# Kernel optimization log

Hardware: AMD Instinct MI355X
Metric: run time of the kernel (lower is better)

Reference implementation:

```python
import jax, jax.numpy as jnp
import numpy as np

NB_CLASSES = 10
NB_NEIGHBORS = 75  # 1 closest + 74 precomputed geodesic neighbors


def setup_inputs() -> dict:
    key = jax.random.key(0)
    k0, k1, k2, k3, k4, k5 = jax.random.split(key, 6)
    nb_data, nb_train, d = 1024, 100000, 256
    x = jax.random.normal(k0, (nb_data, d), dtype=jnp.float32)
    X = jax.random.normal(k1, (nb_train, d), dtype=jnp.float32)
    # train table is stored normalized + centered (init_nn_querier)
    X = X / jnp.linalg.norm(X, axis=1, keepdims=True)
    X = X - jnp.mean(X, axis=0)
    center = jax.random.normal(k2, (d,), dtype=jnp.float32) * 0.01
    train_labels = jax.random.randint(k3, (nb_train,), 0, NB_CLASSES).astype(jnp.int32)
    train_neighbor_index = jax.random.randint(
        k4, (nb_train, NB_NEIGHBORS - 1), 0, nb_train).astype(jnp.int32)
    cali_nonconformity = jnp.sort(
        jax.random.randint(k5, (1000,), 0, NB_NEIGHBORS)).astype(jnp.int32)
    return {
        "x": x, "X": X, "center": center,
        "train_labels": train_labels,
        "train_neighbor_index": train_neighbor_index,
        "cali_nonconformity": cali_nonconformity,
    }


def reference(x, X, center, train_labels, train_neighbor_index, cali_nonconformity):
    # --- find_train_knns: normalize query, center, closest-neighbor search ---
    xq = x / jnp.linalg.norm(x, axis=1, keepdims=True) - center  # [B, d]
    # squared euclidean distances to every train point: [B, nb_train]
    d2 = (jnp.sum(xq * xq, axis=1, keepdims=True)
          - 2.0 * (xq @ X.T)
          + jnp.sum(X * X, axis=1)[None, :])
    closest = jnp.argmin(d2, axis=1)                               # [B]
    # neighbor list = closest point prepended to its precomputed table row
    neigh = jnp.concatenate(
        [closest[:, None], train_neighbor_index[closest]], axis=1)  # [B, K]
    knns_labels = train_labels[neigh]                              # [B, K]
    # --- nonconformity: per-class bincount, #knns NOT in class ---
    counts = jnp.sum(jax.nn.one_hot(knns_labels, NB_CLASSES, dtype=jnp.int32),
                     axis=1)                                       # [B, C]
    knns_not_in_class = jnp.sum(counts, axis=1, keepdims=True) - counts
    # --- preds_conf_cred: conformal p-values via bisect_left ---
    nb_cali = cali_nonconformity.shape[0]
    pos = jnp.searchsorted(cali_nonconformity, knns_not_in_class, side='left')
    p_value = (nb_cali - pos).astype(jnp.float32) / float(nb_cali)  # [B, C]
    preds = jnp.argmax(p_value, axis=1)                             # [B]
    top2, _ = jax.lax.top_k(p_value, 2)                             # [B, 2]
    nb_data = p_value.shape[0]
    creds = jnp.zeros_like(p_value).at[jnp.arange(nb_data), preds].set(top2[:, 0])
    return creds
```

## Files before the change

### kernel.cpp

```cpp
#include <hip/hip_runtime.h>
#include <stdint.h>


typedef __attribute__((ext_vector_type(8))) short short8;
typedef __attribute__((ext_vector_type(4))) float float4v;

static __device__ __forceinline__ unsigned short bf16_rn(float f) {
    unsigned int u = __float_as_uint(f);
    unsigned int r = (u + 0x7FFFu + ((u >> 16) & 1u)) >> 16;
    return (unsigned short)r;
}

static __device__ __forceinline__ void gload_lds16(const void* g, void* l) {
    __builtin_amdgcn_global_load_lds(
        (const __attribute__((address_space(1))) unsigned int*)g,
        (__attribute__((address_space(3))) unsigned int*)l, 16, 0, 0);
}

__global__ void prep_all(const float* __restrict__ X, const float* __restrict__ x,
                         const float* __restrict__ center,
                         unsigned short* __restrict__ Bh, unsigned short* __restrict__ Bl,
                         float* __restrict__ xn2,
                         unsigned short* __restrict__ Ah, unsigned short* __restrict__ Al,
                         float* __restrict__ q2, unsigned long long* __restrict__ gkey,
                         int nb_train, int Np, int B, int Mp) {
    const int tid = threadIdx.x;
    const int tb = Np >> 2;
    if (blockIdx.x < (unsigned)tb) {
        int row = blockIdx.x * 4 + (tid >> 6);
        int lane = tid & 63;
        if (row >= nb_train) {
            ushort4 z = make_ushort4(0, 0, 0, 0);
            *(ushort4*)(Bh + (size_t)row * 256 + lane * 4) = z;
            *(ushort4*)(Bl + (size_t)row * 256 + lane * 4) = z;
            if (lane == 0) xn2[row] = 3.0e38f;
            return;
        }
        float4 v = ((const float4*)(X + (size_t)row * 256))[lane];
        ushort4 h, l;
        h.x = bf16_rn(v.x); l.x = bf16_rn(v.x - __uint_as_float((unsigned)h.x << 16));
        h.y = bf16_rn(v.y); l.y = bf16_rn(v.y - __uint_as_float((unsigned)h.y << 16));
        h.z = bf16_rn(v.z); l.z = bf16_rn(v.z - __uint_as_float((unsigned)h.z << 16));
        h.w = bf16_rn(v.w); l.w = bf16_rn(v.w - __uint_as_float((unsigned)h.w << 16));
        *(ushort4*)(Bh + (size_t)row * 256 + lane * 4) = h;
        *(ushort4*)(Bl + (size_t)row * 256 + lane * 4) = l;
        float ss = v.x * v.x + v.y * v.y + v.z * v.z + v.w * v.w;
        #pragma unroll
        for (int s = 1; s < 64; s <<= 1) ss += __shfl_xor(ss, s);
        if (lane == 0) xn2[row] = ss;
        return;
    }
    int row = blockIdx.x - tb;
    if (row >= Mp) return;
    if (tid == 0) gkey[row] = ~0ULL;
    if (row >= B) {
        Ah[(size_t)row * 256 + tid] = 0;
        Al[(size_t)row * 256 + tid] = 0;
        if (tid == 0) q2[row] = 0.0f;
        return;
    }
    float v = x[(size_t)row * 256 + tid];
    float ss = v * v;
    #pragma unroll
    for (int s = 1; s < 64; s <<= 1) ss += __shfl_xor(ss, s);
    __shared__ float partial[4];
    __shared__ float partial2[4];
    if ((tid & 63) == 0) partial[tid >> 6] = ss;
    __syncthreads();
    float tot = partial[0] + partial[1] + partial[2] + partial[3];
    float inv = 1.0f / sqrtf(tot);
    float val = v * inv - center[tid];
    unsigned short hb = bf16_rn(val);
    float hf = __uint_as_float((unsigned int)hb << 16);
    unsigned short lb = bf16_rn(val - hf);
    Ah[(size_t)row * 256 + tid] = hb;
    Al[(size_t)row * 256 + tid] = lb;
    float ss2 = val * val;
    #pragma unroll
    for (int s = 1; s < 64; s <<= 1) ss2 += __shfl_xor(ss2, s);
    if ((tid & 63) == 0) partial2[tid >> 6] = ss2;
    __syncthreads();
    if (tid == 0) q2[row] = partial2[0] + partial2[1] + partial2[2] + partial2[3];
}

__global__ __launch_bounds__(256, 4) void mfma_tile(
    const unsigned short* __restrict__ Adata,
    const unsigned short* __restrict__ Bdata,
    const float* __restrict__ q2, const float* __restrict__ xn2,
    unsigned long long* __restrict__ gkey,
    int Mp, int Np, int nb_train, int B,
    int ntiles, int nper, int mtiles)
{
    __shared__ unsigned short As[128 * 64];
    __shared__ unsigned short Bs[128 * 64];
    __shared__ unsigned long long skey[128];

    const int bid = blockIdx.x;
    const int xcd = bid & 7;
    const int s_  = bid >> 3;
    const int n_t = xcd * nper + (s_ / mtiles);
    const int m_t = s_ - (s_ / mtiles) * mtiles;
    if (n_t >= ntiles) return;
    const int mtile = m_t * 128;
    const int ntile = n_t * 128;

    const int tid  = threadIdx.x;
    const int wave = tid >> 6;
    const int lane = tid & 63;

    if (tid < 128) skey[tid] = ~0ULL;

    const int isB   = wave >> 1;
    const int Rwave = (wave & 1) * 64;
    const int lrow8  = lane >> 3;
    const int lchunk = lane & 7;
    const size_t APROD = (size_t)Mp * 256;
    const size_t BPROD = (size_t)Np * 256;
    const unsigned short* sbase = isB
        ? (Bdata + (size_t)(ntile + Rwave + lrow8) * 256 + (size_t)((lchunk ^ lrow8) * 8))
        : (Adata + (size_t)(mtile + Rwave + lrow8) * 256 + (size_t)((lchunk ^ lrow8) * 8));
    unsigned short* lwave = (isB ? Bs : As) + Rwave * 64;

    const int mq = (wave >> 1) * 64;
    const int nq = (wave & 1) * 64;
    const int lrow = lane & 15;
    const int kseg = lane >> 4;
    const int sw = lrow & 7;

    float4v acc[4][4];
    #pragma unroll
    for (int i = 0; i < 4; ++i)
        #pragma unroll
        for (int j = 0; j < 4; ++j)
            acc[i][j] = (float4v){0.f, 0.f, 0.f, 0.f};

    for (int s = 0; s < 12; ++s) {
        const int phase = s >> 2;
        const int sk = (s & 3) * 64;
        size_t srcOff = (size_t)sk;
        if (!isB) { if (phase == 1) srcOff += APROD; }
        else      { if (phase == 2) srcOff += BPROD; }
        const unsigned short* g = sbase + srcOff;
        __syncthreads();
        #pragma unroll
        for (int q = 0; q < 8; ++q)
            gload_lds16(g + q * 2048, lwave + q * 512);
        __syncthreads();
        #pragma unroll
        for (int t = 0; t < 2; ++t) {
            const int wch = ((t * 4 + kseg) ^ sw) * 8;
            short8 a[4], b[4];
            #pragma unroll
            for (int i = 0; i < 4; ++i)
                a[i] = *(const short8*)&As[(mq + i * 16 + lrow) * 64 + wch];
            #pragma unroll
            for (int j = 0; j < 4; ++j)
                b[j] = *(const short8*)&Bs[(nq + j * 16 + lrow) * 64 + wch];
            #pragma unroll
            for (int i = 0; i < 4; ++i)
                #pragma unroll
                for (int j = 0; j < 4; ++j)
                    acc[i][j] = __builtin_amdgcn_mfma_f32_16x16x32_bf16(
                        a[i], b[j], acc[i][j], 0, 0, 0);
        }
    }

    float xnv[4];
    #pragma unroll
    for (int j = 0; j < 4; ++j)
        xnv[j] = xn2[ntile + nq + j * 16 + lrow];

    #pragma unroll
    for (int i = 0; i < 4; ++i) {
        #pragma unroll
        for (int r = 0; r < 4; ++r) {
            const int lm = mq + i * 16 + kseg * 4 + r;
            const int mi = mtile + lm;
            unsigned long long best = ~0ULL;
            if (mi < B) {
                float q2v = q2[mi];
                #pragma unroll
                for (int j = 0; j < 4; ++j) {
                    int t_ = ntile + nq + j * 16 + lrow;
                    float sc = fmaxf(q2v - 2.0f * acc[i][j][r] + xnv[j], 0.0f);
                    unsigned long long key =
                        ((unsigned long long)__float_as_uint(sc) << 32) | (unsigned int)t_;
                    best = (key < best) ? key : best;
                }
            }
            #pragma unroll
            for (int sft = 1; sft < 16; sft <<= 1) {
                unsigned long long o = __shfl_xor(best, sft);
                best = (o < best) ? o : best;
            }
            if (lrow == 0 && mi < B) atomicMin(&skey[lm], best);
        }
    }
    __syncthreads();
    if (tid < 128) {
        int mi = mtile + tid;
        if (mi < B && skey[tid] != ~0ULL) atomicMin(gkey + mi, skey[tid]);
    }
}

__global__ void classify(const unsigned long long* __restrict__ gkey,
                         const int* __restrict__ labels,
                         const int* __restrict__ nbr,
                         const int* __restrict__ cali,
                         float* __restrict__ out,
                         int knm1, int nb_cali, int B)
{
    int q = blockIdx.x * 4 + (threadIdx.x >> 6);
    int lane = threadIdx.x & 63;
    if (q >= B) return;
    int closest = (int)(gkey[q] & 0xFFFFFFFFULL);
    int K = knm1 + 1;
    int lbl0 = -1, lbl1 = -1;
    if (lane < K) {
        int idx = (lane == 0) ? closest : nbr[(size_t)closest * knm1 + (lane - 1)];
        lbl0 = labels[idx];
    }
    int j2 = lane + 64;
    if (j2 < K) {
        int idx = nbr[(size_t)closest * knm1 + (j2 - 1)];
        lbl1 = labels[idx];
    }
    int bestc = 0, bestp = -1;
    #pragma unroll
    for (int c = 0; c < 10; ++c) {
        int cnt = __popcll(__ballot(lbl0 == c)) + __popcll(__ballot(lbl1 == c));
        int v = K - cnt;
        int lo = 0, hi = nb_cali;
        while (lo < hi) {
            int mid = (lo + hi) >> 1;
            if (cali[mid] < v) lo = mid + 1; else hi = mid;
        }
        int p = nb_cali - lo;
        if (p > bestp) { bestp = p; bestc = c; }
    }
    float pv = (float)bestp / (float)nb_cali;
    if (lane < 10)
        out[(size_t)q * 10 + lane] = (lane == bestc) ? pv : 0.0f;
}

extern "C" void kernel_launch(void* const* d_in, const int* in_sizes, int n_in,
                              void* d_out, int out_size, void* d_ws, size_t ws_size,
                              hipStream_t stream) {
    const float* x      = (const float*)d_in[0];
    const float* X      = (const float*)d_in[1];
    const float* center = (const float*)d_in[2];
    const int* labels   = (const int*)d_in[3];
    const int* nbr      = (const int*)d_in[4];
    const int* cali     = (const int*)d_in[5];
    float* out = (float*)d_out;

    const int d        = in_sizes[2];
    const int B        = in_sizes[0] / d;
    const int nb_train = in_sizes[3];
    const int knm1     = in_sizes[4] / nb_train;
    const int nb_cali  = in_sizes[5];

    const int Mp = (B + 127) & ~127;
    const int Np = (nb_train + 127) & ~127;

    char* ws = (char*)d_ws;
    size_t off = 0;
    unsigned long long* gkey = (unsigned long long*)(ws + off); off += (size_t)Mp * 8;
    unsigned short* Adata = (unsigned short*)(ws + off); off += (size_t)Mp * 256 * 2 * 2;
    float* q2 = (float*)(ws + off); off += (size_t)Mp * 4;
    unsigned short* Bdata = (unsigned short*)(ws + off); off += (size_t)Np * 256 * 2 * 2;
    float* xn2 = (float*)(ws + off); off += (size_t)Np * 4;

    unsigned short* Ah = Adata;
    unsigned short* Al = Adata + (size_t)Mp * 256;
    unsigned short* Bh = Bdata;
    unsigned short* Bl = Bdata + (size_t)Np * 256;

    prep_all<<<Np / 4 + Mp, 256, 0, stream>>>(X, x, center, Bh, Bl, xn2,
                                              Ah, Al, q2, gkey,
                                              nb_train, Np, B, Mp);
    const int ntiles = Np / 128;
    const int mtiles = Mp / 128;
    const int nper   = (ntiles + 7) / 8;
    mfma_tile<<<8 * nper * mtiles, 256, 0, stream>>>(
        Adata, Bdata, q2, xn2, gkey, Mp, Np, nb_train, B, ntiles, nper, mtiles);
    classify<<<(B + 3) / 4, 256, 0, stream>>>(gkey, labels, nbr, cali, out,
                                              knm1, nb_cali, B);
}
```

Before: 378.6 us.

## Rework distance GEMM into 256x256 tiles with double-buffered LDS pipeline

The MFMA distance kernel moves from 128x128 tiles with 256 threads to 256x256 tiles with 512 threads. Global-to-LDS loads are double-buffered and interleaved with MFMA phases using explicit waitcnt, barriers and setprio, so that memory traffic overlaps compute and each loaded operand is reused more. The M dimension is hardwired to four 256-row tiles, which only covers batches of up to 1024 queries. The roughly 128KB of LDS per block limits occupancy.

```diff
diff --git a/kernel.cpp b/kernel.cpp
--- a/kernel.cpp
+++ b/kernel.cpp
@@ -4,6 +4,11 @@
 
 typedef __attribute__((ext_vector_type(8))) short short8;
 typedef __attribute__((ext_vector_type(4))) float float4v;
+
+#define BAR()   asm volatile("s_barrier" ::: "memory")
+#define LGKM0() asm volatile("s_waitcnt lgkmcnt(0)" ::: "memory")
+#define VMC6()  asm volatile("s_waitcnt vmcnt(6)" ::: "memory")
+#define VMC0()  asm volatile("s_waitcnt vmcnt(0)" ::: "memory")
 
 static __device__ __forceinline__ unsigned short bf16_rn(float f) {
     unsigned int u = __float_as_uint(f);
@@ -83,106 +88,137 @@
     if (tid == 0) q2[row] = partial2[0] + partial2[1] + partial2[2] + partial2[3];
 }
 
-__global__ __launch_bounds__(256, 4) void mfma_tile(
+__global__ __launch_bounds__(512, 2) void mfma_tile(
     const unsigned short* __restrict__ Adata,
     const unsigned short* __restrict__ Bdata,
     const float* __restrict__ q2, const float* __restrict__ xn2,
     unsigned long long* __restrict__ gkey,
-    int Mp, int Np, int nb_train, int B,
-    int ntiles, int nper, int mtiles)
+    int Mp, int Np, int B, int ntiles)
 {
-    __shared__ unsigned short As[128 * 64];
-    __shared__ unsigned short Bs[128 * 64];
-    __shared__ unsigned long long skey[128];
-
-    const int bid = blockIdx.x;
-    const int xcd = bid & 7;
-    const int s_  = bid >> 3;
-    const int n_t = xcd * nper + (s_ / mtiles);
-    const int m_t = s_ - (s_ / mtiles) * mtiles;
-    if (n_t >= ntiles) return;
-    const int mtile = m_t * 128;
-    const int ntile = n_t * 128;
+    __shared__ unsigned short As[2][256 * 64];
+    __shared__ unsigned short Bs[2][256 * 64];
+
+    const int nwg  = ntiles * 4;
+    const int orig = blockIdx.x;
+    const int xcd  = orig & 7;
+    const int qq   = nwg >> 3, rr = nwg & 7;
+    const int wgid = (xcd < rr ? xcd * (qq + 1) : rr * (qq + 1) + (xcd - rr) * qq)
+                   + (orig >> 3);
+    const int mtile = (wgid & 3) * 256;
+    const int ntile = (wgid >> 2) * 256;
 
     const int tid  = threadIdx.x;
     const int wave = tid >> 6;
     const int lane = tid & 63;
-
-    if (tid < 128) skey[tid] = ~0ULL;
-
-    const int isB   = wave >> 1;
-    const int Rwave = (wave & 1) * 64;
-    const int lrow8  = lane >> 3;
-    const int lchunk = lane & 7;
     const size_t APROD = (size_t)Mp * 256;
     const size_t BPROD = (size_t)Np * 256;
-    const unsigned short* sbase = isB
-        ? (Bdata + (size_t)(ntile + Rwave + lrow8) * 256 + (size_t)((lchunk ^ lrow8) * 8))
-        : (Adata + (size_t)(mtile + Rwave + lrow8) * 256 + (size_t)((lchunk ^ lrow8) * 8));
-    unsigned short* lwave = (isB ? Bs : As) + Rwave * 64;
-
-    const int mq = (wave >> 1) * 64;
-    const int nq = (wave & 1) * 64;
-    const int lrow = lane & 15;
-    const int kseg = lane >> 4;
-    const int sw = lrow & 7;
-
-    float4v acc[4][4];
-    #pragma unroll
-    for (int i = 0; i < 4; ++i)
+
+    const int    srow = lane >> 3;
+    const int    schk = ((lane & 7) ^ srow) * 8;
+    const size_t aoff = (size_t)(mtile + wave * 8 + srow) * 256 + schk;
+    const size_t boff = (size_t)(ntile + wave * 8 + srow) * 256 + schk;
+    const int    dwav = wave * 512;
+
+    auto stageA = [&](int tt, int hh) {
+        if (tt >= 12) return;
+        const int p = tt >> 2, sk = (tt & 3) * 64;
+        const unsigned short* src = Adata + (p == 1 ? APROD : 0)
+                                  + aoff + (size_t)hh * (128 * 256) + sk;
+        unsigned short* dst = &As[tt & 1][hh * 8192 + dwav];
+        gload_lds16(src, dst);
+        gload_lds16(src + 64 * 256, dst + 4096);
+    };
+    auto stageB = [&](int tt, int hh) {
+        if (tt >= 12) return;
+        const int p = tt >> 2, sk = (tt & 3) * 64;
+        const unsigned short* src = Bdata + (p == 2 ? BPROD : 0)
+                                  + boff + (size_t)hh * (128 * 256) + sk;
+        unsigned short* dst = &Bs[tt & 1][hh * 8192 + dwav];
+        gload_lds16(src, dst);
+        gload_lds16(src + 64 * 256, dst + 4096);
+    };
+
+    const int wm = wave >> 2, wn = wave & 3;
+    const int lrow = lane & 15, kseg = lane >> 4, sw = lane & 7;
+    const int AM = wm * 128, BN = wn * 64;
+
+    float4v acc[8][4];
+    #pragma unroll
+    for (int i = 0; i < 8; ++i)
         #pragma unroll
         for (int j = 0; j < 4; ++j)
             acc[i][j] = (float4v){0.f, 0.f, 0.f, 0.f};
 
-    for (int s = 0; s < 12; ++s) {
-        const int phase = s >> 2;
-        const int sk = (s & 3) * 64;
-        size_t srcOff = (size_t)sk;
-        if (!isB) { if (phase == 1) srcOff += APROD; }
-        else      { if (phase == 2) srcOff += BPROD; }
-        const unsigned short* g = sbase + srcOff;
-        __syncthreads();
-        #pragma unroll
-        for (int q = 0; q < 8; ++q)
-            gload_lds16(g + q * 2048, lwave + q * 512);
-        __syncthreads();
-        #pragma unroll
-        for (int t = 0; t < 2; ++t) {
-            const int wch = ((t * 4 + kseg) ^ sw) * 8;
-            short8 a[4], b[4];
-            #pragma unroll
-            for (int i = 0; i < 4; ++i)
-                a[i] = *(const short8*)&As[(mq + i * 16 + lrow) * 64 + wch];
-            #pragma unroll
-            for (int j = 0; j < 4; ++j)
-                b[j] = *(const short8*)&Bs[(nq + j * 16 + lrow) * 64 + wch];
-            #pragma unroll
-            for (int i = 0; i < 4; ++i)
-                #pragma unroll
-                for (int j = 0; j < 4; ++j)
-                    acc[i][j] = __builtin_amdgcn_mfma_f32_16x16x32_bf16(
-                        a[i], b[j], acc[i][j], 0, 0, 0);
-        }
-    }
+    short8 a[4][2], bA[2][2], bB[2][2];
+    const unsigned short* Ab;
+    const unsigned short* Bb;
+
+#define RDA(h) { _Pragma("unroll") for (int i = 0; i < 4; ++i) \
+                 _Pragma("unroll") for (int t = 0; t < 2; ++t) \
+    a[i][t] = *(const short8*)&Ab[(AM + (h)*64 + i*16 + lrow)*64 + (((t*4+kseg)^sw)*8)]; }
+#define RDB(dst, j0) { _Pragma("unroll") for (int j = 0; j < 2; ++j) \
+                       _Pragma("unroll") for (int t = 0; t < 2; ++t) \
+    dst[j][t] = *(const short8*)&Bb[(BN + ((j0)+j)*16 + lrow)*64 + (((t*4+kseg)^sw)*8)]; }
+#define MF(h, bf, j0) { _Pragma("unroll") for (int t = 0; t < 2; ++t) \
+                        _Pragma("unroll") for (int i = 0; i < 4; ++i) \
+                        _Pragma("unroll") for (int j = 0; j < 2; ++j) \
+    acc[(h)*4+i][(j0)+j] = __builtin_amdgcn_mfma_f32_16x16x32_bf16( \
+        a[i][t], bf[j][t], acc[(h)*4+i][(j0)+j], 0, 0, 0); }
+
+    stageA(0, 0); stageA(0, 1); stageB(0, 0); stageB(0, 1);
+    stageB(1, 0); stageB(1, 1); stageA(1, 0);
+    VMC6(); BAR();
+
+    int cur = 0;
+    for (int m = 0; m < 12; ++m) {
+        Ab = As[cur]; Bb = Bs[cur];
+        RDA(0); RDB(bA, 0);
+        stageA(m + 1, 1);
+        BAR(); LGKM0();
+        __builtin_amdgcn_s_setprio(1); MF(0, bA, 0); __builtin_amdgcn_s_setprio(0);
+        BAR();
+        RDB(bB, 2);
+        BAR(); LGKM0();
+        __builtin_amdgcn_s_setprio(1); MF(0, bB, 2); __builtin_amdgcn_s_setprio(0);
+        BAR();
+        RDA(1);
+        stageB(m + 2, 0);
+        BAR(); LGKM0();
+        __builtin_amdgcn_s_setprio(1); MF(1, bB, 2); __builtin_amdgcn_s_setprio(0);
+        BAR();
+        stageB(m + 2, 1); stageA(m + 2, 0);
+        BAR();
+        __builtin_amdgcn_s_setprio(1); MF(1, bA, 0); __builtin_amdgcn_s_setprio(0);
+        if (m < 10) { VMC6(); } else { VMC0(); }
+        BAR();
+        cur ^= 1;
+    }
+#undef RDA
+#undef RDB
+#undef MF
+
+    unsigned long long* skey = (unsigned long long*)&As[0][0];
+    if (tid < 256) skey[tid] = ~0ULL;
+    __syncthreads();
 
     float xnv[4];
     #pragma unroll
     for (int j = 0; j < 4; ++j)
-        xnv[j] = xn2[ntile + nq + j * 16 + lrow];
-
-    #pragma unroll
-    for (int i = 0; i < 4; ++i) {
+        xnv[j] = xn2[ntile + BN + j * 16 + lrow];
+
+    #pragma unroll
+    for (int mi = 0; mi < 8; ++mi) {
         #pragma unroll
         for (int r = 0; r < 4; ++r) {
-            const int lm = mq + i * 16 + kseg * 4 + r;
-            const int mi = mtile + lm;
+            const int lm = AM + mi * 16 + kseg * 4 + r;
+            const int gm = mtile + lm;
             unsigned long long best = ~0ULL;
-            if (mi < B) {
-                float q2v = q2[mi];
+            if (gm < B) {
+                float q2v = q2[gm];
                 #pragma unroll
                 for (int j = 0; j < 4; ++j) {
-                    int t_ = ntile + nq + j * 16 + lrow;
-                    float sc = fmaxf(q2v - 2.0f * acc[i][j][r] + xnv[j], 0.0f);
+                    int t_ = ntile + BN + j * 16 + lrow;
+                    float sc = fmaxf(q2v - 2.0f * acc[mi][j][r] + xnv[j], 0.0f);
                     unsigned long long key =
                         ((unsigned long long)__float_as_uint(sc) << 32) | (unsigned int)t_;
                     best = (key < best) ? key : best;
@@ -193,13 +229,13 @@
                 unsigned long long o = __shfl_xor(best, sft);
                 best = (o < best) ? o : best;
             }
-            if (lrow == 0 && mi < B) atomicMin(&skey[lm], best);
+            if (lrow == 0 && gm < B) atomicMin(&skey[lm], best);
         }
     }
     __syncthreads();
-    if (tid < 128) {
-        int mi = mtile + tid;
-        if (mi < B && skey[tid] != ~0ULL) atomicMin(gkey + mi, skey[tid]);
+    if (tid < 256) {
+        int gm = mtile + tid;
+        if (gm < B && skey[tid] != ~0ULL) atomicMin(gkey + gm, skey[tid]);
     }
 }
 
@@ -260,8 +296,8 @@
     const int knm1     = in_sizes[4] / nb_train;
     const int nb_cali  = in_sizes[5];
 
-    const int Mp = (B + 127) & ~127;
-    const int Np = (nb_train + 127) & ~127;
+    const int Mp = (B + 255) & ~255;
+    const int Np = (nb_train + 255) & ~255;
 
     char* ws = (char*)d_ws;
     size_t off = 0;
@@ -279,11 +315,9 @@
     prep_all<<<Np / 4 + Mp, 256, 0, stream>>>(X, x, center, Bh, Bl, xn2,
                                               Ah, Al, q2, gkey,
                                               nb_train, Np, B, Mp);
-    const int ntiles = Np / 128;
-    const int mtiles = Mp / 128;
-    const int nper   = (ntiles + 7) / 8;
-    mfma_tile<<<8 * nper * mtiles, 256, 0, stream>>>(
-        Adata, Bdata, q2, xn2, gkey, Mp, Np, nb_train, B, ntiles, nper, mtiles);
+    const int ntiles = Np / 256;
+    mfma_tile<<<ntiles * 4, 512, 0, stream>>>(
+        Adata, Bdata, q2, xn2, gkey, Mp, Np, B, ntiles);
     classify<<<(B + 3) / 4, 256, 0, stream>>>(gkey, labels, nbr, cali, out,
                                               knm1, nb_cali, B);
 }
```

Result: slower. 400.8 us (+5.9%).
